# Kernel tuning notes

Measured on AMD Instinct MI355X. Metric: run time of the kernel, lower is better.

The kernel has to match this reference:

```python
import jax, jax.numpy as jnp
import numpy as np

N_QUBITS = 4
N_LAYERS = 2
ENT = [(i, (i + 1) % N_QUBITS) for i in range(N_QUBITS)]  # fixed entangling ring


def _ry(t):
    c, s = jnp.cos(t / 2), jnp.sin(t / 2)
    return jnp.stack([jnp.stack([c, -s]), jnp.stack([s, c])]).astype(jnp.complex64)


def _rx(t):
    c, s = jnp.cos(t / 2), jnp.sin(t / 2)
    return jnp.stack([jnp.stack([c + 0j, -1j * s]), jnp.stack([-1j * s, c + 0j])]).astype(jnp.complex64)


def _rz(t):
    e = jnp.exp(-0.5j * t.astype(jnp.complex64))
    z = jnp.zeros_like(e)
    return jnp.stack([jnp.stack([e, z]), jnp.stack([z, jnp.conj(e)])])


def _apply_1q(state, U, w):
    # state: (2,)*N_QUBITS; apply 2x2 U on wire w
    s = jnp.moveaxis(state, w, 0)
    s = jnp.tensordot(U, s, ((1,), (0,)))
    return jnp.moveaxis(s, 0, w)


def _cnot(state, c, t):
    s = jnp.moveaxis(state, (c, t), (0, 1))
    s = jnp.concatenate([s[:1], jnp.flip(s[1:], axis=1)], axis=0)
    return jnp.moveaxis(s, (0, 1), (c, t))


def _ansatz(state, vec, params):
    for i in range(N_QUBITS):
        state = _apply_1q(state, _ry(vec[i]), i)
    for l in range(N_LAYERS):
        for i in range(N_QUBITS):
            state = _apply_1q(state, _rx(params[l, i, 0]), i)
            state = _apply_1q(state, _ry(params[l, i, 1]), i)
            state = _apply_1q(state, _rz(params[l, i, 2]), i)
        for a_, b_ in ENT:
            state = _cnot(state, a_, b_)
    return state


def _adjoint_ansatz(state, vec, params):
    # inverse gates in reverse order
    for l in reversed(range(N_LAYERS)):
        for a_, b_ in reversed(ENT):
            state = _cnot(state, a_, b_)  # CNOT is self-inverse
        for i in reversed(range(N_QUBITS)):
            state = _apply_1q(state, _rz(-params[l, i, 2]), i)
            state = _apply_1q(state, _ry(-params[l, i, 1]), i)
            state = _apply_1q(state, _rx(-params[l, i, 0]), i)
    for i in reversed(range(N_QUBITS)):
        state = _apply_1q(state, _ry(-vec[i]), i)
    return state


def setup_inputs() -> dict:
    key = jax.random.key(0)
    k1, k2, k3 = jax.random.split(key, 3)
    a = jax.random.normal(k1, (1024, N_QUBITS), dtype=jnp.float32)
    b = jax.random.normal(k2, (1024, N_QUBITS), dtype=jnp.float32)
    params = jax.random.normal(k3, (N_LAYERS, N_QUBITS, 3), dtype=jnp.float32)
    return {"a": a, "b": b, "params": params}


def reference(a, b, params):
    def pair(x, y):
        psi = jnp.zeros((2,) * N_QUBITS, jnp.complex64).at[(0,) * N_QUBITS].set(1.0)
        psi = _ansatz(psi, x, params)
        psi = _adjoint_ansatz(psi, y, params)
        probs = jnp.abs(psi) ** 2
        # expval of PauliZ on wire 0: +1 for |0>, -1 for |1> on axis 0
        z = jnp.sum(probs[0]) - jnp.sum(probs[1])
        return jnp.abs(z)

    # Gram matrix [len(a), len(b)]
    return jax.vmap(lambda x: jax.vmap(lambda y: pair(x, y))(b))(a)
```

## Files before the change

### kernel.cpp

```cpp
#include <hip/hip_runtime.h>


#define NA 1024
#define NB 1024
#define KDIM 512

typedef __attribute__((ext_vector_type(8))) short bf16x8;
typedef __attribute__((ext_vector_type(4))) float f32x4;

__device__ __forceinline__ unsigned short f2bf(float x) {
    union { float f; unsigned u; } v; v.f = x;
    unsigned r = v.u + 0x7fffu + ((v.u >> 16) & 1u);
    return (unsigned short)(r >> 16);
}

__device__ __forceinline__ uint4 pack8(const float* f) {
    uint4 u;
    u.x = (unsigned)f2bf(f[0]) | ((unsigned)f2bf(f[1]) << 16);
    u.y = (unsigned)f2bf(f[2]) | ((unsigned)f2bf(f[3]) << 16);
    u.z = (unsigned)f2bf(f[4]) | ((unsigned)f2bf(f[5]) << 16);
    u.w = (unsigned)f2bf(f[6]) | ((unsigned)f2bf(f[7]) << 16);
    return u;
}

__device__ __forceinline__ void ry_gate(float* sr, float* si, int w, float t) {
    float s, c; __sincosf(0.5f * t, &s, &c);
    int st = 8 >> w;
    #pragma unroll
    for (int b = 0; b < 16; ++b) {
        if (b & st) continue;
        int j = b | st;
        float r0 = sr[b], i0 = si[b], r1 = sr[j], i1 = si[j];
        sr[b] = c * r0 - s * r1;  si[b] = c * i0 - s * i1;
        sr[j] = s * r0 + c * r1;  si[j] = s * i0 + c * i1;
    }
}

__device__ __forceinline__ void rx_gate(float* sr, float* si, int w, float t) {
    float s, c; __sincosf(0.5f * t, &s, &c);
    int st = 8 >> w;
    #pragma unroll
    for (int b = 0; b < 16; ++b) {
        if (b & st) continue;
        int j = b | st;
        float r0 = sr[b], i0 = si[b], r1 = sr[j], i1 = si[j];
        sr[b] = c * r0 + s * i1;  si[b] = c * i0 - s * r1;
        sr[j] = c * r1 + s * i0;  si[j] = c * i1 - s * r0;
    }
}

__device__ __forceinline__ void rz_gate(float* sr, float* si, int w, float t) {
    float s, c; __sincosf(0.5f * t, &s, &c);
    int st = 8 >> w;
    #pragma unroll
    for (int b = 0; b < 16; ++b) {
        if (b & st) continue;
        int j = b | st;
        float r0 = sr[b], i0 = si[b], r1 = sr[j], i1 = si[j];
        sr[b] = c * r0 + s * i0;  si[b] = c * i0 - s * r0;
        sr[j] = c * r1 - s * i1;  si[j] = c * i1 + s * r1;
    }
}

__device__ __forceinline__ void cnot_gate(float* sr, float* si, int cw, int tw) {
    int cs = 8 >> cw, ts = 8 >> tw;
    #pragma unroll
    for (int b = 0; b < 16; ++b) {
        if ((b & cs) && !(b & ts)) {
            int j = b | ts;
            float tr = sr[b]; sr[b] = sr[j]; sr[j] = tr;
            float ti = si[b]; si[b] = si[j]; si[j] = ti;
        }
    }
}

__device__ __forceinline__ void ansatz(float* sr, float* si, const float* vec, const float* P) {
    #pragma unroll
    for (int q = 0; q < 4; ++q) ry_gate(sr, si, q, vec[q]);
    #pragma unroll
    for (int l = 0; l < 2; ++l) {
        #pragma unroll
        for (int q = 0; q < 4; ++q) {
            rx_gate(sr, si, q, P[l * 12 + q * 3 + 0]);
            ry_gate(sr, si, q, P[l * 12 + q * 3 + 1]);
            rz_gate(sr, si, q, P[l * 12 + q * 3 + 2]);
        }
        cnot_gate(sr, si, 0, 1);
        cnot_gate(sr, si, 1, 2);
        cnot_gate(sr, si, 2, 3);
        cnot_gate(sr, si, 3, 0);
    }
}

__global__ __launch_bounds__(64) void qkm_phase1(
    const float* __restrict__ a, const float* __restrict__ b,
    const float* __restrict__ params,
    uint4* __restrict__ Qv, uint4* __restrict__ Mv) {
    float P[24];
    #pragma unroll
    for (int j = 0; j < 24; ++j) P[j] = params[j];
    int tid = threadIdx.x;
    int blk = blockIdx.x;

    if (blk < 256) {
        __shared__ float vr[4][16][17];
        __shared__ float vi[4][16][17];
        int yl = tid >> 4, p = tid & 15;
        int y = (blk << 2) + yl;
        float sr[16], si[16];
        #pragma unroll
        for (int k = 0; k < 16; ++k) { sr[k] = (k == p) ? 1.f : 0.f; si[k] = 0.f; }
        float vec[4];
        #pragma unroll
        for (int q = 0; q < 4; ++q) vec[q] = b[y * 4 + q];
        ansatz(sr, si, vec, P);
        #pragma unroll
        for (int k = 0; k < 16; ++k) { vr[yl][p][k] = sr[k]; vi[yl][p][k] = si[k]; }
        __syncthreads();
        int k = p;
        float mr[16], mi[16];
        #pragma unroll
        for (int l = 0; l < 16; ++l) { mr[l] = 0.f; mi[l] = 0.f; }
        #pragma unroll
        for (int p2 = 0; p2 < 16; ++p2) {
            float d = (p2 & 8) ? -1.f : 1.f;
            float ar = vr[yl][p2][k], ai = vi[yl][p2][k];
            float dar = d * ar, dai = d * ai;
            #pragma unroll
            for (int l = 0; l < 16; ++l) {
                float br = vr[yl][p2][l], bi = vi[yl][p2][l];
                mr[l] += dar * br + dai * bi;
                mi[l] += dai * br - dar * bi;
            }
        }
        float ni[16];
        #pragma unroll
        for (int l = 0; l < 16; ++l) ni[l] = -mi[l];
        uint4* d0 = Mv + y * 64 + k * 2;
        d0[0] = pack8(&mr[0]); d0[1] = pack8(&mr[8]);
        uint4* d1 = Mv + y * 64 + 32 + k * 2;
        d1[0] = pack8(&ni[0]); d1[1] = pack8(&ni[8]);
    } else {
        int i = ((blk - 256) << 6) + tid;
        float sr[16], si[16];
        #pragma unroll
        for (int k = 0; k < 16; ++k) { sr[k] = (k == 0) ? 1.f : 0.f; si[k] = 0.f; }
        float vec[4];
        #pragma unroll
        for (int q = 0; q < 4; ++q) vec[q] = a[i * 4 + q];
        ansatz(sr, si, vec, P);
        #pragma unroll
        for (int k = 0; k < 16; ++k) {
            float t0[16], t1[16];
            float rk = sr[k], ik = si[k];
            #pragma unroll
            for (int l = 0; l < 16; ++l) {
                t0[l] = rk * sr[l] + ik * si[l];
                t1[l] = rk * si[l] - ik * sr[l];
            }
            uint4* d0 = Qv + i * 64 + k * 2;
            d0[0] = pack8(t0); d0[1] = pack8(t0 + 8);
            uint4* d1 = Qv + i * 64 + 32 + k * 2;
            d1[0] = pack8(t1); d1[1] = pack8(t1 + 8);
        }
    }
}

__global__ __launch_bounds__(256) void qkm_phase2(
    const unsigned short* __restrict__ Q, const unsigned short* __restrict__ M,
    float* __restrict__ out) {
    int wave = threadIdx.x >> 6;
    int lane = threadIdx.x & 63;
    int bi = blockIdx.x >> 5;
    int bj = blockIdx.x & 31;
    int wi = wave >> 1, wj = wave & 1;
    int row0 = bi * 32 + wi * 16;
    int col0 = bj * 32 + wj * 16;
    int m16 = lane & 15;
    int quad = lane >> 4;

    const unsigned short* qrow = Q + (row0 + m16) * KDIM + quad * 8;
    const unsigned short* mrow = M + (col0 + m16) * KDIM + quad * 8;

    f32x4 acc = {0.f, 0.f, 0.f, 0.f};
    #pragma unroll
    for (int kk = 0; kk < 16; ++kk) {
        bf16x8 afrag = *(const bf16x8*)(qrow + kk * 32);
        bf16x8 bfrag = *(const bf16x8*)(mrow + kk * 32);
        acc = __builtin_amdgcn_mfma_f32_16x16x32_bf16(afrag, bfrag, acc, 0, 0, 0);
    }
    #pragma unroll
    for (int r = 0; r < 4; ++r) {
        int orow = row0 + quad * 4 + r;
        int ocol = col0 + m16;
        out[orow * NB + ocol] = fabsf(acc[r]);
    }
}

extern "C" void kernel_launch(void* const* d_in, const int* in_sizes, int n_in,
                              void* d_out, int out_size, void* d_ws, size_t ws_size,
                              hipStream_t stream) {
    const float* a = (const float*)d_in[0];
    const float* b = (const float*)d_in[1];
    const float* params = (const float*)d_in[2];
    float* out = (float*)d_out;

    unsigned short* Q = (unsigned short*)d_ws;
    unsigned short* M = Q + (size_t)NA * KDIM;

    qkm_phase1<<<256 + NA / 64, 64, 0, stream>>>(a, b, params, (uint4*)Q, (uint4*)M);
    qkm_phase2<<<(NA / 32) * (NB / 32), 256, 0, stream>>>(Q, M, out);
}
```

Measured before the change: 83.08 us.

## Enlarge GEMM tiles with 2x2 MFMA per wave, XCD-aware block mapping, vectorized LDS

Phase 2 now has each wave compute a 32x32 output tile with four MFMAs that reuse the loaded Q and M fragments, so each block covers 64x64 and the grid drops from 1024 to 256 blocks. Blocks are remapped so that consecutive blocks sharing an XCD (blk & 7) work on the same two row tiles, which should improve L2 locality. Phase 1 stores the per-y state in a padded flat LDS layout and reads it with float4 loads to cut the number of LDS instructions. The trade-off is fewer blocks and higher register pressure per wave, which lowers parallelism.

```diff
diff --git a/kernel.cpp b/kernel.cpp
--- a/kernel.cpp
+++ b/kernel.cpp
@@ -103,8 +103,7 @@
     int blk = blockIdx.x;
 
     if (blk < 256) {
-        __shared__ float vr[4][16][17];
-        __shared__ float vi[4][16][17];
+        __shared__ float V[4 * 520];
         int yl = tid >> 4, p = tid & 15;
         int y = (blk << 2) + yl;
         float sr[16], si[16];
@@ -114,8 +113,12 @@
         #pragma unroll
         for (int q = 0; q < 4; ++q) vec[q] = b[y * 4 + q];
         ansatz(sr, si, vec, P);
-        #pragma unroll
-        for (int k = 0; k < 16; ++k) { vr[yl][p][k] = sr[k]; vi[yl][p][k] = si[k]; }
+        float* row = &V[yl * 520 + p * 32];
+        #pragma unroll
+        for (int c = 0; c < 4; ++c) {
+            *(float4*)(row + 4 * c)      = *(float4*)(sr + 4 * c);
+            *(float4*)(row + 16 + 4 * c) = *(float4*)(si + 4 * c);
+        }
         __syncthreads();
         int k = p;
         float mr[16], mi[16];
@@ -123,14 +126,18 @@
         for (int l = 0; l < 16; ++l) { mr[l] = 0.f; mi[l] = 0.f; }
         #pragma unroll
         for (int p2 = 0; p2 < 16; ++p2) {
+            const float* r2 = &V[yl * 520 + p2 * 32];
             float d = (p2 & 8) ? -1.f : 1.f;
-            float ar = vr[yl][p2][k], ai = vi[yl][p2][k];
+            float ar = r2[k], ai = r2[16 + k];
             float dar = d * ar, dai = d * ai;
             #pragma unroll
-            for (int l = 0; l < 16; ++l) {
-                float br = vr[yl][p2][l], bi = vi[yl][p2][l];
-                mr[l] += dar * br + dai * bi;
-                mi[l] += dai * br - dar * bi;
+            for (int c = 0; c < 4; ++c) {
+                float4 brv = *(const float4*)(r2 + 4 * c);
+                float4 biv = *(const float4*)(r2 + 16 + 4 * c);
+                mr[c*4+0] += dar * brv.x + dai * biv.x;  mi[c*4+0] += dai * brv.x - dar * biv.x;
+                mr[c*4+1] += dar * brv.y + dai * biv.y;  mi[c*4+1] += dai * brv.y - dar * biv.y;
+                mr[c*4+2] += dar * brv.z + dai * biv.z;  mi[c*4+2] += dai * brv.z - dar * biv.z;
+                mr[c*4+3] += dar * brv.w + dai * biv.w;  mi[c*4+3] += dai * brv.w - dar * biv.w;
             }
         }
         float ni[16];
@@ -171,29 +178,43 @@
     float* __restrict__ out) {
     int wave = threadIdx.x >> 6;
     int lane = threadIdx.x & 63;
-    int bi = blockIdx.x >> 5;
-    int bj = blockIdx.x & 31;
+    int blk = blockIdx.x;
+    int xcd = blk & 7;
+    int slot = blk >> 3;
+    int bi = xcd * 2 + (slot >> 4);
+    int bj = slot & 15;
     int wi = wave >> 1, wj = wave & 1;
-    int row0 = bi * 32 + wi * 16;
-    int col0 = bj * 32 + wj * 16;
+    int row0 = bi * 64 + wi * 32;
+    int col0 = bj * 64 + wj * 32;
     int m16 = lane & 15;
     int quad = lane >> 4;
 
-    const unsigned short* qrow = Q + (row0 + m16) * KDIM + quad * 8;
-    const unsigned short* mrow = M + (col0 + m16) * KDIM + quad * 8;
-
-    f32x4 acc = {0.f, 0.f, 0.f, 0.f};
-    #pragma unroll
+    const unsigned short* q0 = Q + (size_t)(row0 + m16) * KDIM + quad * 8;
+    const unsigned short* q1 = q0 + 16 * KDIM;
+    const unsigned short* m0 = M + (size_t)(col0 + m16) * KDIM + quad * 8;
+    const unsigned short* m1 = m0 + 16 * KDIM;
+
+    f32x4 a00 = {0.f,0.f,0.f,0.f}, a01 = {0.f,0.f,0.f,0.f};
+    f32x4 a10 = {0.f,0.f,0.f,0.f}, a11 = {0.f,0.f,0.f,0.f};
+    #pragma unroll 4
     for (int kk = 0; kk < 16; ++kk) {
-        bf16x8 afrag = *(const bf16x8*)(qrow + kk * 32);
-        bf16x8 bfrag = *(const bf16x8*)(mrow + kk * 32);
-        acc = __builtin_amdgcn_mfma_f32_16x16x32_bf16(afrag, bfrag, acc, 0, 0, 0);
+        bf16x8 qa = *(const bf16x8*)(q0 + kk * 32);
+        bf16x8 qb = *(const bf16x8*)(q1 + kk * 32);
+        bf16x8 ma = *(const bf16x8*)(m0 + kk * 32);
+        bf16x8 mb = *(const bf16x8*)(m1 + kk * 32);
+        a00 = __builtin_amdgcn_mfma_f32_16x16x32_bf16(qa, ma, a00, 0, 0, 0);
+        a01 = __builtin_amdgcn_mfma_f32_16x16x32_bf16(qa, mb, a01, 0, 0, 0);
+        a10 = __builtin_amdgcn_mfma_f32_16x16x32_bf16(qb, ma, a10, 0, 0, 0);
+        a11 = __builtin_amdgcn_mfma_f32_16x16x32_bf16(qb, mb, a11, 0, 0, 0);
     }
     #pragma unroll
     for (int r = 0; r < 4; ++r) {
-        int orow = row0 + quad * 4 + r;
-        int ocol = col0 + m16;
-        out[orow * NB + ocol] = fabsf(acc[r]);
+        int r0o = row0 + quad * 4 + r;
+        int r1o = r0o + 16;
+        out[r0o * NB + col0 + m16]      = fabsf(a00[r]);
+        out[r0o * NB + col0 + 16 + m16] = fabsf(a01[r]);
+        out[r1o * NB + col0 + m16]      = fabsf(a10[r]);
+        out[r1o * NB + col0 + 16 + m16] = fabsf(a11[r]);
     }
 }
 
@@ -209,5 +230,5 @@
     unsigned short* M = Q + (size_t)NA * KDIM;
 
     qkm_phase1<<<256 + NA / 64, 64, 0, stream>>>(a, b, params, (uint4*)Q, (uint4*)M);
-    qkm_phase2<<<(NA / 32) * (NB / 32), 256, 0, stream>>>(Q, M, out);
-}
+    qkm_phase2<<<256, 256, 0, stream>>>(Q, M, out);
+}
```

Measured after the change: 75.65 us. 8.9% less time.
